# Kernel optimization log

Hardware: AMD Instinct MI355X
Metric: run time of the kernel (lower is better)

The kernel has to match this reference:

```python
import jax, jax.numpy as jnp
import numpy as np


def setup_inputs() -> dict:
    key = jax.random.key(0)
    k1, k2 = jax.random.split(key)
    b, c, h, w = 32, 3, 32, 32
    N = 100000
    x = jax.random.normal(k1, (b, c, h, w), dtype=jnp.float32)
    train_data = jax.random.normal(k2, (N, c, h, w), dtype=jnp.float32)
    # linear beta schedule (diffusion default): betas in [1e-4, 0.02], T=1000
    betas = jnp.linspace(1e-4, 0.02, 1000, dtype=jnp.float32)
    alphas_cumprod = jnp.cumprod(1.0 - betas)
    t = 150  # t_start < t < t_end branch -> epsilon_star_batch
    return {"x": x, "train_data": train_data, "alphas_cumprod": alphas_cumprod, "t": t}


def reference(x, train_data, alphas_cumprod, t):
    # epsilon_star_batch: softmax-weighted average of train set under
    # Gaussian kernel exp(-||x - sqrt(ab)*x0||^2 / (2*(1-ab)))
    ab = alphas_cumprod[t]
    s = jnp.sqrt(ab)
    one_minus = 1.0 - ab
    b = x.shape[0]
    N = train_data.shape[0]
    xf = x.reshape(b, -1)            # [b, D]
    tf = train_data.reshape(N, -1)   # [N, D]
    # ||x - s*x0||^2 = ||x||^2 - 2 s x.x0 + s^2 ||x0||^2 (avoids [b,N,D] blowup)
    x_sq = jnp.sum(xf * xf, axis=1, keepdims=True)      # [b,1]
    t_sq = jnp.sum(tf * tf, axis=1)                     # [N]
    cross = xf @ tf.T                                   # [b,N]
    logits = -(x_sq - 2.0 * s * cross + ab * t_sq) / (2.0 * one_minus)  # [b,N]
    wts = jax.nn.softmax(logits, axis=1)                # [b,N]
    weighted_x = (wts @ tf).reshape(x.shape)            # [b,c,h,w]
    inv = 1.0 / jnp.sqrt(one_minus)
    return x * inv - s * inv * weighted_x
```

## Files before the change

kernel.cpp:

```cpp
#include <hip/hip_runtime.h>

#define BATCH  32
#define DIM    3072
#define NTRAIN 100000

#define KCH    128
#define NCH    24
#define ROWB   528
#define BUFB   (32 * ROWB)

#define NSEG   8
#define SEGJ   12500
#define SEGCAP 1024
#define THRESH 25.0f

typedef __bf16 bf16x8 __attribute__((ext_vector_type(8)));
typedef float  f32x16 __attribute__((ext_vector_type(16)));
typedef unsigned short u16;
typedef unsigned int   u32;

union F8 { u16 us[8]; u32 ui[4]; uint4 u4; bf16x8 bf; };

__device__ __forceinline__ u16   bft(float f){ return (u16)(__float_as_uint(f) >> 16); }
__device__ __forceinline__ float bfh(float f){ return __uint_as_float(__float_as_uint(f) & 0xFFFF0000u); }

__global__ __launch_bounds__(256) void k0_split_x_v2(
        const float* __restrict__ x, u16* __restrict__ xfh, u16* __restrict__ xfl) {
    int task = blockIdx.x * 256 + threadIdx.x;
    if (task >= 12288) return;
    int kb  = task >> 6;
    int rem = task & 63;
    int r   = rem >> 1;
    int g   = rem & 1;
    const float* src = x + r * DIM + kb * 16 + g * 8;
    float4 A = *(const float4*)(src);
    float4 B = *(const float4*)(src + 4);
    float fv[8] = {A.x, A.y, A.z, A.w, B.x, B.y, B.z, B.w};
    F8 h, l;
#pragma unroll
    for (int e = 0; e < 8; ++e) {
        h.us[e] = bft(fv[e]);
        l.us[e] = bft(fv[e] - bfh(fv[e]));
    }
    size_t off = (size_t)kb * 512 + r * 16 + g * 8;
    *(uint4*)(xfh + off) = h.u4;
    *(uint4*)(xfl + off) = l.u4;
}

__global__ __launch_bounds__(256) void k1_logits_v6(
        const float* __restrict__ train,
        const u16* __restrict__ xfh, const u16* __restrict__ xfl,
        const float* __restrict__ alphas, const int* __restrict__ tptr,
        float* __restrict__ logits) {
    __shared__ __align__(16) char smem[3 * BUFB];
    const int tid  = threadIdx.x;
    const int lane = tid & 63;
    const int w    = tid >> 6;
    const int l31  = lane & 31;
    const int g    = lane >> 5;
    const int jt0  = blockIdx.x * 32;

    const float ab = alphas[tptr[0]];
    const float s  = sqrtf(ab);
    const float om = 1.0f - ab;
    const float c1 = s / om;
    const float c2 = ab / (2.0f * om);

    const char* gblk = (const char*)train + (size_t)jt0 * (DIM * 4);

    f32x16 acc;
#pragma unroll
    for (int r = 0; r < 16; ++r) acc[r] = 0.0f;
    float tsqp = 0.0f;

    auto stage = [&](int buf, int c) {
        if (lane < 32) {
#pragma unroll
            for (int i = 0; i < 8; ++i) {
                const int r = w * 8 + i;
                const char* src = gblk + (size_t)r * (DIM * 4) + c * (KCH * 4) + lane * 16;
                char* dst = smem + buf * BUFB + r * ROWB;
                __builtin_amdgcn_global_load_lds(
                    (const __attribute__((address_space(1))) unsigned int*)src,
                    (__attribute__((address_space(3))) unsigned int*)dst,
                    16, 0, 0);
            }
        }
    };
    auto ldx = [&](int c, F8* ah, F8* al) {
#pragma unroll
        for (int s4 = 0; s4 < 2; ++s4) {
            const int kb16 = c * 8 + w * 2 + s4;
            const size_t off = (size_t)kb16 * 512 + l31 * 16 + g * 8;
            ah[s4].u4 = *(const uint4*)(xfh + off);
            al[s4].u4 = *(const uint4*)(xfl + off);
        }
    };

    F8 ahc[2], alc[2];
    stage(0, 0);
    __builtin_amdgcn_sched_barrier(0);
    ldx(0, ahc, alc);
    __builtin_amdgcn_sched_barrier(0);
    stage(1, 1);

    for (int c = 0; c < NCH; ++c) {
        if (c < NCH - 1) {
            asm volatile("s_waitcnt vmcnt(8)\n\ts_barrier" ::: "memory");
        } else {
            asm volatile("s_waitcnt vmcnt(0)\n\ts_barrier" ::: "memory");
        }

        F8 ahn[2], aln[2];
        if (c + 1 < NCH) ldx(c + 1, ahn, aln);
        __builtin_amdgcn_sched_barrier(0);
        if (c + 2 < NCH) stage((c + 2) % 3, c + 2);
        __builtin_amdgcn_sched_barrier(0);

        const char* lb = smem + (c % 3) * BUFB + l31 * ROWB;
#pragma unroll
        for (int s4 = 0; s4 < 2; ++s4) {
            const u32 kb0 = (u32)(w * 128 + s4 * 64 + g * 32);
            const float4 f0 = *(const float4*)(lb + kb0);
            const float4 f1 = *(const float4*)(lb + kb0 + 16);
            float fv[8] = {f0.x, f0.y, f0.z, f0.w, f1.x, f1.y, f1.z, f1.w};
            F8 bh, bl;
#pragma unroll
            for (int e = 0; e < 8; ++e) {
                float f = fv[e];
                bh.us[e] = bft(f);
                bl.us[e] = bft(f - bfh(f));
                tsqp = fmaf(f, f, tsqp);
            }
            acc = __builtin_amdgcn_mfma_f32_32x32x16_bf16(ahc[s4].bf, bh.bf, acc, 0, 0, 0);
            acc = __builtin_amdgcn_mfma_f32_32x32x16_bf16(alc[s4].bf, bh.bf, acc, 0, 0, 0);
            acc = __builtin_amdgcn_mfma_f32_32x32x16_bf16(ahc[s4].bf, bl.bf, acc, 0, 0, 0);
        }
        if (c + 1 < NCH) {
            ahc[0] = ahn[0]; ahc[1] = ahn[1];
            alc[0] = aln[0]; alc[1] = aln[1];
        }
    }
    __syncthreads();

    tsqp += __shfl_xor(tsqp, 32);
    float* red = (float*)smem;
    if (w > 0) {
        float* dp = red + ((w - 1) * 64 + lane) * 16;
#pragma unroll
        for (int r = 0; r < 16; ++r) dp[r] = acc[r];
    }
    if (g == 0) red[3072 + w * 32 + l31] = tsqp;
    __syncthreads();
    if (w == 0) {
#pragma unroll
        for (int q = 0; q < 3; ++q) {
            const float* sp = red + (q * 64 + lane) * 16;
#pragma unroll
            for (int r = 0; r < 16; ++r) acc[r] += sp[r];
        }
        const float tsq = red[3072 + l31] + red[3072 + 32 + l31]
                        + red[3072 + 64 + l31] + red[3072 + 96 + l31];
#pragma unroll
        for (int r = 0; r < 16; ++r) {
            int brow = (r & 3) + 8 * (r >> 2) + 4 * g;
            logits[(size_t)brow * NTRAIN + jt0 + l31] = c1 * acc[r] - c2 * tsq;
        }
    }
}

__global__ __launch_bounds__(256) void k2a_rowmax(
        const float* __restrict__ logits, float* __restrict__ m_part) {
    const int b   = blockIdx.x >> 3;
    const int seg = blockIdx.x & 7;
    const int j0  = seg * SEGJ;
    const int j1  = min(j0 + SEGJ, NTRAIN);
    const float* row = logits + (size_t)b * NTRAIN;
    float mx = -3.0e38f;
    for (int j = j0 + threadIdx.x; j < j1; j += 256) mx = fmaxf(mx, row[j]);
    __shared__ float red[256];
    red[threadIdx.x] = mx;
    __syncthreads();
    for (int off = 128; off > 0; off >>= 1) {
        if (threadIdx.x < (unsigned)off)
            red[threadIdx.x] = fmaxf(red[threadIdx.x], red[threadIdx.x + off]);
        __syncthreads();
    }
    if (threadIdx.x == 0) m_part[blockIdx.x] = red[0];
}

__global__ __launch_bounds__(256) void k2b_select(
        const float* __restrict__ logits, const float* __restrict__ m_part,
        int* __restrict__ idx, float* __restrict__ wts,
        int* __restrict__ cnt, float* __restrict__ lsum) {
    const int b   = blockIdx.x >> 3;
    const int seg = blockIdx.x & 7;
    const int tid = threadIdx.x;
    float mb = -3.0e38f;
#pragma unroll
    for (int sg = 0; sg < NSEG; ++sg) mb = fmaxf(mb, m_part[b * NSEG + sg]);
    const int j0 = seg * SEGJ;
    const int j1 = min(j0 + SEGJ, NTRAIN);
    const float* lrow = logits + (size_t)b * NTRAIN;

    int mycnt = 0;
    for (int j = j0 + tid; j < j1; j += 256)
        if (lrow[j] >= mb - THRESH) ++mycnt;

    __shared__ int   soff[257];
    __shared__ float ssum[256];
    soff[tid + 1] = mycnt;
    __syncthreads();
    if (tid == 0) {
        soff[0] = 0;
        for (int t = 1; t <= 256; ++t) soff[t] += soff[t - 1];
    }
    __syncthreads();

    int off = soff[tid];
    const int base = (b * NSEG + seg) * SEGCAP;
    float mysum = 0.0f;
    for (int j = j0 + tid; j < j1; j += 256) {
        float lg = lrow[j];
        if (lg >= mb - THRESH) {
            float wv = __expf(lg - mb);
            mysum += wv;
            if (off < SEGCAP) { idx[base + off] = j; wts[base + off] = wv; }
            ++off;
        }
    }
    ssum[tid] = mysum;
    __syncthreads();
    if (tid == 0) {
        float Ls = 0.0f;
        for (int t = 0; t < 256; ++t) Ls += ssum[t];
        lsum[b * NSEG + seg] = Ls;
        cnt[b * NSEG + seg]  = min(soff[256], SEGCAP);
    }
}

__global__ __launch_bounds__(256) void k3_gather(
        const float* __restrict__ x, const float* __restrict__ train,
        const int* __restrict__ idx, const float* __restrict__ wts,
        const int* __restrict__ cnt, const float* __restrict__ lsum,
        const float* __restrict__ alphas, const int* __restrict__ tptr,
        float* __restrict__ out) {
    const int blk  = blockIdx.x;
    const int b    = blk / 12;
    const int dseg = blk % 12;
    const int d    = dseg * 256 + threadIdx.x;

    const float ab  = alphas[tptr[0]];
    const float s   = sqrtf(ab);
    const float om  = 1.0f - ab;
    const float inv = 1.0f / sqrtf(om);

    float L = 0.0f;
#pragma unroll
    for (int sg = 0; sg < NSEG; ++sg) L += lsum[b * NSEG + sg];

    float acc = 0.0f;
    for (int sg = 0; sg < NSEG; ++sg) {
        const int n    = cnt[b * NSEG + sg];
        const int base = (b * NSEG + sg) * SEGCAP;
        for (int i = 0; i < n; ++i) {
            const int   j = idx[base + i];
            const float w = wts[base + i];
            acc = fmaf(w, train[(size_t)j * DIM + d], acc);
        }
    }
    const size_t o = (size_t)b * DIM + d;
    out[o] = inv * x[o] - s * inv * (acc / L);
}

extern "C" void kernel_launch(void* const* d_in, const int* in_sizes, int n_in,
                              void* d_out, int out_size, void* d_ws, size_t ws_size,
                              hipStream_t stream) {
    const float* x      = (const float*)d_in[0];
    const float* train  = (const float*)d_in[1];
    const float* alphas = (const float*)d_in[2];
    const int*   tptr   = (const int*)d_in[3];
    float* out = (float*)d_out;

    char* ws = (char*)d_ws;
    float* logits = (float*)ws;
    float* m_part = (float*)(ws + 12800000);
    float* lsum   = (float*)(ws + 12801024);
    int*   cnt    = (int*)(ws + 12802048);
    int*   idx    = (int*)(ws + 12803072);
    float* wts    = (float*)(ws + 13851648);
    u16*   xfh    = (u16*)(ws + 14900224);
    u16*   xfl    = (u16*)(ws + 15096832);

    k0_split_x_v2<<<48, 256, 0, stream>>>(x, xfh, xfl);
    k1_logits_v6<<<NTRAIN / 32, 256, 0, stream>>>(train, xfh, xfl, alphas, tptr, logits);
    k2a_rowmax<<<BATCH * NSEG, 256, 0, stream>>>(logits, m_part);
    k2b_select<<<BATCH * NSEG, 256, 0, stream>>>(logits, m_part, idx, wts, cnt, lsum);
    k3_gather<<<BATCH * 12, 256, 0, stream>>>(x, train, idx, wts, cnt, lsum,
                                              alphas, tptr, out);
}
```

Measured before the change: 315.8 us.

## Fuse per-block row max into logits kernel and XOR-swizzle LDS staging

The logits kernel now computes a per-block max across its 32 train columns for each batch row and writes it to a partials array. The row-max kernel then reduces those 3125 partials per row rather than rescanning the whole 12.8 MB logits buffer. Staging also changes: all 64 lanes issue loads for two rows per call, padding is dropped, and an XOR swizzle avoids LDS bank conflicts, halving load instructions per wave. This adds shuffle reductions to the logits epilogue and changes the vmcnt wait count.

```diff
diff --git a/kernel.cpp b/kernel.cpp
--- a/kernel.cpp
+++ b/kernel.cpp
@@ -3,16 +3,18 @@
 #define BATCH  32
 #define DIM    3072
 #define NTRAIN 100000
+#define NBLK1  3125
 
 #define KCH    128
 #define NCH    24
-#define ROWB   528
+#define ROWB   512
 #define BUFB   (32 * ROWB)
 
 #define NSEG   8
 #define SEGJ   12500
 #define SEGCAP 1024
 #define THRESH 25.0f
+#define MPROW  3136
 
 typedef __bf16 bf16x8 __attribute__((ext_vector_type(8)));
 typedef float  f32x16 __attribute__((ext_vector_type(16)));
@@ -47,11 +49,11 @@
     *(uint4*)(xfl + off) = l.u4;
 }
 
-__global__ __launch_bounds__(256) void k1_logits_v6(
+__global__ __launch_bounds__(256) void k1_logits_v7(
         const float* __restrict__ train,
         const u16* __restrict__ xfh, const u16* __restrict__ xfl,
         const float* __restrict__ alphas, const int* __restrict__ tptr,
-        float* __restrict__ logits) {
+        float* __restrict__ logits, float* __restrict__ m_part) {
     __shared__ __align__(16) char smem[3 * BUFB];
     const int tid  = threadIdx.x;
     const int lane = tid & 63;
@@ -74,17 +76,17 @@
     float tsqp = 0.0f;
 
     auto stage = [&](int buf, int c) {
-        if (lane < 32) {
-#pragma unroll
-            for (int i = 0; i < 8; ++i) {
-                const int r = w * 8 + i;
-                const char* src = gblk + (size_t)r * (DIM * 4) + c * (KCH * 4) + lane * 16;
-                char* dst = smem + buf * BUFB + r * ROWB;
-                __builtin_amdgcn_global_load_lds(
-                    (const __attribute__((address_space(1))) unsigned int*)src,
-                    (__attribute__((address_space(3))) unsigned int*)dst,
-                    16, 0, 0);
-            }
+#pragma unroll
+        for (int i = 0; i < 4; ++i) {
+            const int R0 = w * 8 + i * 2;
+            const int r  = R0 + (lane >> 5);
+            const u32 colS = (u32)((lane & 31) << 4) ^ ((u32)(r & 7) << 4);
+            const char* src = gblk + (size_t)r * (DIM * 4) + c * (KCH * 4) + colS;
+            char* dst = smem + buf * BUFB + R0 * ROWB;
+            __builtin_amdgcn_global_load_lds(
+                (const __attribute__((address_space(1))) unsigned int*)src,
+                (__attribute__((address_space(3))) unsigned int*)dst,
+                16, 0, 0);
         }
     };
     auto ldx = [&](int c, F8* ah, F8* al) {
@@ -104,9 +106,11 @@
     __builtin_amdgcn_sched_barrier(0);
     stage(1, 1);
 
+    const u32 rsw = ((u32)(l31 & 7)) << 4;
+
     for (int c = 0; c < NCH; ++c) {
         if (c < NCH - 1) {
-            asm volatile("s_waitcnt vmcnt(8)\n\ts_barrier" ::: "memory");
+            asm volatile("s_waitcnt vmcnt(4)\n\ts_barrier" ::: "memory");
         } else {
             asm volatile("s_waitcnt vmcnt(0)\n\ts_barrier" ::: "memory");
         }
@@ -121,8 +125,8 @@
 #pragma unroll
         for (int s4 = 0; s4 < 2; ++s4) {
             const u32 kb0 = (u32)(w * 128 + s4 * 64 + g * 32);
-            const float4 f0 = *(const float4*)(lb + kb0);
-            const float4 f1 = *(const float4*)(lb + kb0 + 16);
+            const float4 f0 = *(const float4*)(lb + ((kb0      ) ^ rsw));
+            const float4 f1 = *(const float4*)(lb + ((kb0 + 16u) ^ rsw));
             float fv[8] = {f0.x, f0.y, f0.z, f0.w, f1.x, f1.y, f1.z, f1.w};
             F8 bh, bl;
 #pragma unroll
@@ -161,23 +165,34 @@
         }
         const float tsq = red[3072 + l31] + red[3072 + 32 + l31]
                         + red[3072 + 64 + l31] + red[3072 + 96 + l31];
+        float lg[16];
 #pragma unroll
         for (int r = 0; r < 16; ++r) {
+            lg[r] = c1 * acc[r] - c2 * tsq;
             int brow = (r & 3) + 8 * (r >> 2) + 4 * g;
-            logits[(size_t)brow * NTRAIN + jt0 + l31] = c1 * acc[r] - c2 * tsq;
-        }
-    }
-}
-
-__global__ __launch_bounds__(256) void k2a_rowmax(
-        const float* __restrict__ logits, float* __restrict__ m_part) {
-    const int b   = blockIdx.x >> 3;
-    const int seg = blockIdx.x & 7;
-    const int j0  = seg * SEGJ;
-    const int j1  = min(j0 + SEGJ, NTRAIN);
-    const float* row = logits + (size_t)b * NTRAIN;
+            logits[(size_t)brow * NTRAIN + jt0 + l31] = lg[r];
+        }
+#pragma unroll
+        for (int d = 1; d < 32; d <<= 1)
+#pragma unroll
+            for (int r = 0; r < 16; ++r)
+                lg[r] = fmaxf(lg[r], __shfl_xor(lg[r], d));
+        if (l31 == 0) {
+#pragma unroll
+            for (int r = 0; r < 16; ++r) {
+                int brow = (r & 3) + 8 * (r >> 2) + 4 * g;
+                m_part[(size_t)brow * MPROW + blockIdx.x] = lg[r];
+            }
+        }
+    }
+}
+
+__global__ __launch_bounds__(256) void k2a_rowmax_v2(
+        const float* __restrict__ m_part, float* __restrict__ m) {
+    const int b = blockIdx.x;
     float mx = -3.0e38f;
-    for (int j = j0 + threadIdx.x; j < j1; j += 256) mx = fmaxf(mx, row[j]);
+    for (int i = threadIdx.x; i < NBLK1; i += 256)
+        mx = fmaxf(mx, m_part[(size_t)b * MPROW + i]);
     __shared__ float red[256];
     red[threadIdx.x] = mx;
     __syncthreads();
@@ -186,19 +201,17 @@
             red[threadIdx.x] = fmaxf(red[threadIdx.x], red[threadIdx.x + off]);
         __syncthreads();
     }
-    if (threadIdx.x == 0) m_part[blockIdx.x] = red[0];
+    if (threadIdx.x == 0) m[b] = red[0];
 }
 
 __global__ __launch_bounds__(256) void k2b_select(
-        const float* __restrict__ logits, const float* __restrict__ m_part,
+        const float* __restrict__ logits, const float* __restrict__ m,
         int* __restrict__ idx, float* __restrict__ wts,
         int* __restrict__ cnt, float* __restrict__ lsum) {
     const int b   = blockIdx.x >> 3;
     const int seg = blockIdx.x & 7;
     const int tid = threadIdx.x;
-    float mb = -3.0e38f;
-#pragma unroll
-    for (int sg = 0; sg < NSEG; ++sg) mb = fmaxf(mb, m_part[b * NSEG + sg]);
+    const float mb = m[b];
     const int j0 = seg * SEGJ;
     const int j1 = min(j0 + SEGJ, NTRAIN);
     const float* lrow = logits + (size_t)b * NTRAIN;
@@ -285,17 +298,19 @@
     char* ws = (char*)d_ws;
     float* logits = (float*)ws;
     float* m_part = (float*)(ws + 12800000);
-    float* lsum   = (float*)(ws + 12801024);
-    int*   cnt    = (int*)(ws + 12802048);
-    int*   idx    = (int*)(ws + 12803072);
-    float* wts    = (float*)(ws + 13851648);
-    u16*   xfh    = (u16*)(ws + 14900224);
-    u16*   xfl    = (u16*)(ws + 15096832);
+    float* m_arr  = (float*)(ws + 13201408);
+    float* lsum   = (float*)(ws + 13201536);
+    int*   cnt    = (int*)(ws + 13202560);
+    int*   idx    = (int*)(ws + 13203584);
+    float* wts    = (float*)(ws + 14252160);
+    u16*   xfh    = (u16*)(ws + 15300736);
+    u16*   xfl    = (u16*)(ws + 15497344);
 
     k0_split_x_v2<<<48, 256, 0, stream>>>(x, xfh, xfl);
-    k1_logits_v6<<<NTRAIN / 32, 256, 0, stream>>>(train, xfh, xfl, alphas, tptr, logits);
-    k2a_rowmax<<<BATCH * NSEG, 256, 0, stream>>>(logits, m_part);
-    k2b_select<<<BATCH * NSEG, 256, 0, stream>>>(logits, m_part, idx, wts, cnt, lsum);
+    k1_logits_v7<<<NBLK1, 256, 0, stream>>>(train, xfh, xfl, alphas, tptr,
+                                            logits, m_part);
+    k2a_rowmax_v2<<<BATCH, 256, 0, stream>>>(m_part, m_arr);
+    k2b_select<<<BATCH * NSEG, 256, 0, stream>>>(logits, m_arr, idx, wts, cnt, lsum);
     k3_gather<<<BATCH * 12, 256, 0, stream>>>(x, train, idx, wts, cnt, lsum,
                                               alphas, tptr, out);
 }
```

New measurement: 305.9 us. -3.1%, faster.
